# Performance work log

Hardware: AMD Instinct MI355X
Metric: run time of the kernel (lower is better)

## Reference

```python
import jax, jax.numpy as jnp
import numpy as np

B, S, D = 2, 2048, 1024
H, DH = 16, 64
LN_EPS = 1e-5
NEG_INF = -1e9


def setup_inputs() -> dict:
    key = jax.random.key(0)
    ks = jax.random.split(key, 8)
    x = jax.random.normal(ks[0], (B, S, D), dtype=jnp.float32)
    mask = jax.random.randint(ks[1], (B, 1, S, S), 0, 5) == 0
    sc = 1.0 / np.sqrt(D)
    W_attn = jax.random.normal(ks[2], (D, 3 * H * DH), dtype=jnp.float32) * sc
    b_attn = jnp.zeros((3 * H * DH,), dtype=jnp.float32)
    W_out = jax.random.normal(ks[3], (H * DH, D), dtype=jnp.float32) * sc
    b_out = jnp.zeros((D,), dtype=jnp.float32)
    ln_g = jnp.ones((D,), dtype=jnp.float32)
    ln_b = jnp.zeros((D,), dtype=jnp.float32)
    return {"x": x, "W_attn": W_attn, "b_attn": b_attn, "W_out": W_out,
            "b_out": b_out, "ln_g": ln_g, "ln_b": ln_b, "mask": mask}


def reference(x, W_attn, b_attn, W_out, b_out, ln_g, ln_b, mask):
    bs, s, _ = x.shape
    qkv = x @ W_attn + b_attn                      # [b, s, 3*H*DH]
    q, k, v = jnp.split(qkv, 3, axis=-1)
    q = q.reshape(bs, s, H, DH)
    k = k.reshape(bs, s, H, DH)
    v = v.reshape(bs, s, H, DH)
    scores = jnp.einsum('bqhd,bkhd->bhqk', q, k) / np.sqrt(DH)
    scores = jnp.where(mask, NEG_INF, scores)
    probs = jax.nn.softmax(scores, axis=-1)        # attn_p = 0 -> dropout is identity
    attn = jnp.einsum('bhqk,bkhd->bqhd', probs, v).reshape(bs, s, H * DH)
    y = x + (attn @ W_out + b_out)                 # resid_p = 0
    mu = jnp.mean(y, axis=-1, keepdims=True)
    var = jnp.mean((y - mu) ** 2, axis=-1, keepdims=True)
    return (y - mu) * jax.lax.rsqrt(var + LN_EPS) * ln_g + ln_b
```

## Files before the change

### kernel.cpp

```cpp
#include <hip/hip_runtime.h>
#include <math.h>

#define BB 2
#define SS 2048
#define DD 1024
#define HH 16
#define DHD 64
#define N3 3072
#define LN_EPS 1e-5f

#define PLANE (BB*HH*SS*DHD)

typedef __attribute__((ext_vector_type(8))) short bf16x8;
typedef __attribute__((ext_vector_type(4))) float f32x4;
typedef __attribute__((ext_vector_type(16))) float f32x16;
typedef unsigned int u32;
typedef unsigned short ushort_t;

static __device__ __forceinline__ short f2bf(float f) {
  union { float f; unsigned u; } a;
  a.f = f;
  unsigned r = a.u + 0x7fffu + ((a.u >> 16) & 1u);
  return (short)(r >> 16);
}

static __device__ __forceinline__ u32 fbits(float f) {
  union { float f; u32 u; } a; a.f = f; return a.u;
}

static __device__ __forceinline__ float ex2(float x) {
  float r;
  asm("v_exp_f32 %0, %1" : "=v"(r) : "v"(x));
  return r;
}

static __device__ __forceinline__ u32 pkbf(float lo, float hi) {
  return __builtin_amdgcn_perm(fbits(hi) + 0x8000u, fbits(lo) + 0x8000u,
                               0x07060302u);
}

static __device__ __forceinline__ void gload_lds16(const void* g, void* l) {
  __builtin_amdgcn_global_load_lds(
      (const __attribute__((address_space(1))) u32*)g,
      (__attribute__((address_space(3))) u32*)l, 16, 0, 0);
}

#define PREP_CONV_B   2048
#define PREP_TA_B     768
#define PREP_TO_B     256
#define PREP_PACK_B   32768
#define PREP_TOTAL_B  (PREP_CONV_B + PREP_TA_B + PREP_TO_B + PREP_PACK_B)

__global__ __launch_bounds__(256) void prep_kernel(
    const float* __restrict__ x, ushort_t* __restrict__ xb,
    const float* __restrict__ Wa, ushort_t* __restrict__ watt,
    const float* __restrict__ Wo, ushort_t* __restrict__ wot,
    const int* __restrict__ mask, unsigned long long* __restrict__ bits) {
  __shared__ float tile[64][65];
  const int tid = threadIdx.x;
  const int bid = blockIdx.x;

  if (bid < PREP_CONV_B) {
    int i = (bid * 256 + tid) * 8;
    float4 a = *(const float4*)&x[i];
    float4 b = *(const float4*)&x[i + 4];
    short s[8] = {f2bf(a.x), f2bf(a.y), f2bf(a.z), f2bf(a.w),
                  f2bf(b.x), f2bf(b.y), f2bf(b.z), f2bf(b.w)};
    *(bf16x8*)&xb[i] = *(bf16x8*)s;
    return;
  }
  if (bid < PREP_CONV_B + PREP_TA_B + PREP_TO_B) {
    const float* W; ushort_t* Wt; int K, N, nb, kb;
    if (bid < PREP_CONV_B + PREP_TA_B) {
      int idx = bid - PREP_CONV_B;
      W = Wa; Wt = watt; K = DD; N = N3;
      nb = (idx % 48) * 64; kb = (idx / 48) * 64;
    } else {
      int idx = bid - PREP_CONV_B - PREP_TA_B;
      W = Wo; Wt = wot; K = DD; N = DD;
      nb = (idx % 16) * 64; kb = (idx / 16) * 64;
    }
    #pragma unroll
    for (int i = 0; i < 4; ++i) {
      int idx = tid + i * 256;
      int r = idx >> 4, c = (idx & 15) * 4;
      float4 v = *(const float4*)&W[(size_t)(kb + r) * N + nb + c];
      tile[r][c] = v.x; tile[r][c + 1] = v.y;
      tile[r][c + 2] = v.z; tile[r][c + 3] = v.w;
    }
    __syncthreads();
    #pragma unroll
    for (int i = 0; i < 4; ++i) {
      int idx = tid + i * 256;
      int n = idx >> 4, k = (idx & 15) * 4;
      short4 s;
      s.x = f2bf(tile[k][n]); s.y = f2bf(tile[k + 1][n]);
      s.z = f2bf(tile[k + 2][n]); s.w = f2bf(tile[k + 3][n]);
      *(short4*)&Wt[(size_t)(nb + n) * K + kb + k] = s;
    }
    return;
  }
  {
    size_t g = (size_t)(bid - PREP_CONV_B - PREP_TA_B - PREP_TO_B) * 256 + tid;
    int m = mask[g];
    unsigned long long b = __ballot(m != 0);
    if ((tid & 63) == 0) bits[g >> 6] = b;
  }
}

#define GEMM_MAIN(Aptr, Btptr, Kdim)                                          \
  __shared__ ushort_t As[128 * 64];                                           \
  __shared__ ushort_t Bs[128 * 64];                                           \
  const int tid = threadIdx.x;                                                \
  const int wave = tid >> 6, lane = tid & 63;                                 \
  const int lane16 = lane & 15, quad = lane >> 4;                             \
  const int wm = wave & 1, wn = wave >> 1;                                    \
  const int bm = blockIdx.y * 128, bn = blockIdx.x * 128;                     \
  const int srow = lane >> 3;                                                 \
  const int sg = (lane & 7) ^ srow;                                           \
  f32x4 acc[4][4];                                                            \
  _Pragma("unroll") for (int i = 0; i < 4; ++i)                               \
    _Pragma("unroll") for (int j = 0; j < 4; ++j)                             \
      acc[i][j] = (f32x4){0.f, 0.f, 0.f, 0.f};                                \
  const ushort_t* agp[4];                                                     \
  const ushort_t* bgp[4];                                                     \
  _Pragma("unroll") for (int i = 0; i < 4; ++i) {                             \
    int seg = wave * 4 + i;                                                   \
    int r = seg * 8 + srow;                                                   \
    agp[i] = Aptr + (size_t)(bm + r) * Kdim + sg * 8;                         \
    bgp[i] = Btptr + (size_t)(bn + r) * Kdim + sg * 8;                        \
  }                                                                           \
  for (int k0 = 0; k0 < Kdim; k0 += 64) {                                     \
    _Pragma("unroll") for (int i = 0; i < 4; ++i) {                           \
      int seg = wave * 4 + i;                                                 \
      gload_lds16(agp[i] + k0, &As[seg * 512]);                               \
      gload_lds16(bgp[i] + k0, &Bs[seg * 512]);                               \
    }                                                                         \
    __syncthreads();                                                          \
    _Pragma("unroll") for (int ks = 0; ks < 2; ++ks) {                        \
      bf16x8 af[4], bfr[4];                                                   \
      _Pragma("unroll") for (int mt = 0; mt < 4; ++mt) {                      \
        int ra = wm * 64 + mt * 16 + lane16;                                  \
        int kc = ks * 4 + quad;                                               \
        af[mt] = *(const bf16x8*)&As[ra * 64 + ((kc ^ (ra & 7)) * 8)];        \
      }                                                                       \
      _Pragma("unroll") for (int nt = 0; nt < 4; ++nt) {                      \
        int rb = wn * 64 + nt * 16 + lane16;                                  \
        int kc = ks * 4 + quad;                                               \
        bfr[nt] = *(const bf16x8*)&Bs[rb * 64 + ((kc ^ (rb & 7)) * 8)];       \
      }                                                                       \
      _Pragma("unroll") for (int mt = 0; mt < 4; ++mt)                        \
        _Pragma("unroll") for (int nt = 0; nt < 4; ++nt)                      \
          acc[mt][nt] = __builtin_amdgcn_mfma_f32_16x16x32_bf16(              \
              af[mt], bfr[nt], acc[mt][nt], 0, 0, 0);                         \
    }                                                                         \
    __syncthreads();                                                          \
  }

__global__ __launch_bounds__(256) void gemm_qkv_mfma(
    const ushort_t* __restrict__ A, const ushort_t* __restrict__ Bt,
    const float* __restrict__ bias, ushort_t* __restrict__ qkvh) {
  GEMM_MAIN(A, Bt, DD)
  #pragma unroll
  for (int nt = 0; nt < 4; ++nt) {
    int col = bn + wn * 64 + nt * 16 + lane16;
    int which = col >> 10, hcol = col & 1023;
    int head = hcol >> 6, d = hcol & 63;
    float bv = bias[col];
    ushort_t* plane = qkvh + (size_t)which * PLANE;
    #pragma unroll
    for (int mt = 0; mt < 4; ++mt) {
      #pragma unroll
      for (int reg = 0; reg < 4; ++reg) {
        int row = bm + wm * 64 + mt * 16 + quad * 4 + reg;
        int bb = row >> 11, ss = row & (SS - 1);
        plane[((size_t)(bb * HH + head) * SS + ss) * DHD + d] =
            (ushort_t)f2bf(acc[mt][nt][reg] + bv);
      }
    }
  }
}

__global__ __launch_bounds__(256) void gemm_proj_mfma(
    const ushort_t* __restrict__ A, const ushort_t* __restrict__ Bt,
    const float* __restrict__ bias, const float* __restrict__ xres,
    float* __restrict__ Y) {
  GEMM_MAIN(A, Bt, DD)
  #pragma unroll
  for (int nt = 0; nt < 4; ++nt) {
    int col = bn + wn * 64 + nt * 16 + lane16;
    float bv = bias[col];
    #pragma unroll
    for (int mt = 0; mt < 4; ++mt) {
      #pragma unroll
      for (int reg = 0; reg < 4; ++reg) {
        int row = bm + wm * 64 + mt * 16 + quad * 4 + reg;
        Y[(size_t)row * DD + col] =
            acc[mt][nt][reg] + bv + xres[(size_t)row * DD + col];
      }
    }
  }
}

__global__ __launch_bounds__(256) void vtrans_kernel(
    const ushort_t* __restrict__ vh, ushort_t* __restrict__ vt) {
  __shared__ short t[64][80];
  const int tid = threadIdx.x;
  const int bh = blockIdx.x >> 5;
  const int st = blockIdx.x & 31;
  const size_t hb = (size_t)bh * SS * DHD;
  #pragma unroll
  for (int i = 0; i < 2; ++i) {
    int idx = tid + i * 256;
    int r = idx >> 3, ch = idx & 7;
    bf16x8 v = *(const bf16x8*)&vh[hb + (size_t)(st * 64 + r) * DHD + ch * 8];
    *(bf16x8*)&t[r][ch * 8] = v;
  }
  __syncthreads();
  #pragma unroll
  for (int i = 0; i < 2; ++i) {
    int idx = tid + i * 256;
    int d = idx >> 3, ch = idx & 7;
    short s[8];
    #pragma unroll
    for (int j = 0; j < 8; ++j) s[j] = t[ch * 8 + j][d];
    *(bf16x8*)&vt[hb + (size_t)d * SS + st * 64 + ch * 8] = *(bf16x8*)s;
  }
}

__global__ __launch_bounds__(512, 4) void attn_mfma_kernel(
    const ushort_t* __restrict__ qh, const ushort_t* __restrict__ kh,
    const ushort_t* __restrict__ vt, const u32* __restrict__ mbits,
    ushort_t* __restrict__ attn_out) {
  __shared__ __align__(16) ushort_t S[2][2][2][4096];

  const int tid = threadIdx.x;
  const int wave = tid >> 6, lane = tid & 63;
  const int l31 = lane & 31, hi = lane >> 5;

  const int bh = blockIdx.x & 31;
  const int qt = blockIdx.x >> 5;
  const int bbi = bh >> 4, hhi = bh & 15;
  const size_t head_base = (size_t)bh * SS * DHD;
  const int wq = wave & 3, khx = wave >> 2;
  const int q32 = qt * 128 + wq * 32;
  const int qrow = q32 + l31;

  bf16x8 qf[4];
  {
    const float kScale = 0.125f * 1.44269504f;
    const ushort_t* qsrc = &qh[head_base + (size_t)qrow * DHD + hi * 8];
    #pragma unroll
    for (int dk = 0; dk < 4; ++dk) {
      bf16x8 r = *(const bf16x8*)&qsrc[dk * 16];
      #pragma unroll
      for (int e = 0; e < 8; ++e) {
        union { u32 u; float f; } c;
        c.u = ((u32)(ushort_t)r[e]) << 16;
        c.f *= kScale;
        r[e] = f2bf(c.f);
      }
      qf[dk] = r;
    }
  }

  f32x16 acc0, acc1;
  #pragma unroll
  for (int e = 0; e < 16; ++e) { acc0[e] = 0.f; acc1[e] = 0.f; }
  float lsum = 0.f;

  const u32* mrow = mbits + ((size_t)(bbi * SS) + qrow) * 64 + khx * 32;

  const int sr = tid >> 3;
  const int scsrc = (tid & 7) ^ (sr & 7);
  const ushort_t* kst0 = kh + head_base + (size_t)sr * DHD + scsrc * 8;
  const ushort_t* vst0 = vt + head_base + (size_t)sr * SS + scsrc * 8;
  const int sdst = wave * 512;

#define ATTN_STAGE(buf, t)                                                    \
  gload_lds16(kst0 + (size_t)(t) * 64 * DHD, &S[buf][0][0][sdst]);            \
  gload_lds16(kst0 + (size_t)(1024 + (t) * 64) * DHD, &S[buf][0][1][sdst]);   \
  gload_lds16(vst0 + (t) * 64, &S[buf][1][0][sdst]);                          \
  gload_lds16(vst0 + 1024 + (t) * 64, &S[buf][1][1][sdst]);

  ATTN_STAGE(0, 0);
  uint2 mcur = *(const uint2*)mrow;
  __syncthreads();

  const int NT = 16;
  for (int t = 0; t < NT; ++t) {
    const int cur = t & 1;
    uint2 mnext = mcur;
    if (t + 1 < NT) {
      ATTN_STAGE(cur ^ 1, t + 1);
      mnext = *(const uint2*)&mrow[(t + 1) * 2];
    }

    const ushort_t* Kb = &S[cur][0][khx][0];
    const ushort_t* Vb = &S[cur][1][khx][0];

    f32x16 s0, s1;
    #pragma unroll
    for (int e = 0; e < 16; ++e) { s0[e] = 0.f; s1[e] = 0.f; }
    #pragma unroll
    for (int dk = 0; dk < 4; ++dk) {
      const int c = 2 * dk + hi;
      const int r0 = l31;
      bf16x8 kf0 = *(const bf16x8*)&Kb[r0 * 64 + ((c ^ (r0 & 7)) * 8)];
      s0 = __builtin_amdgcn_mfma_f32_32x32x16_bf16(kf0, qf[dk], s0, 0, 0, 0);
      const int r1 = 32 + l31;
      bf16x8 kf1 = *(const bf16x8*)&Kb[r1 * 64 + ((c ^ (r1 & 7)) * 8)];
      s1 = __builtin_amdgcn_mfma_f32_32x32x16_bf16(kf1, qf[dk], s1, 0, 0, 0);
    }

    #pragma unroll
    for (int ks16 = 0; ks16 < 4; ++ks16) {
      const int ksub = ks16 >> 1;
      const int g0 = (ks16 & 1) * 2;
      const f32x16 sv = ksub ? s1 : s0;
      const u32 w32 = ksub ? mcur.y : mcur.x;
      const u32 na = w32 >> (g0 * 8 + hi * 4);
      const u32 nb = w32 >> (g0 * 8 + 8 + hi * 4);
      float e0 = (na & 1u) ? 0.f : ex2(sv[g0 * 4 + 0]);
      float e1 = (na & 2u) ? 0.f : ex2(sv[g0 * 4 + 1]);
      float e2 = (na & 4u) ? 0.f : ex2(sv[g0 * 4 + 2]);
      float e3 = (na & 8u) ? 0.f : ex2(sv[g0 * 4 + 3]);
      float f0 = (nb & 1u) ? 0.f : ex2(sv[g0 * 4 + 4]);
      float f1 = (nb & 2u) ? 0.f : ex2(sv[g0 * 4 + 5]);
      float f2 = (nb & 4u) ? 0.f : ex2(sv[g0 * 4 + 6]);
      float f3 = (nb & 8u) ? 0.f : ex2(sv[g0 * 4 + 7]);
      lsum += ((e0 + e1) + (e2 + e3)) + ((f0 + f1) + (f2 + f3));
      u32 a0 = pkbf(e0, e1), a1 = pkbf(e2, e3);
      u32 b0 = pkbf(f0, f1), b1 = pkbf(f2, f3);
      asm("v_permlane32_swap_b32 %0, %1" : "+v"(a0), "+v"(b0));
      asm("v_permlane32_swap_b32 %0, %1" : "+v"(a1), "+v"(b1));
      union { u32 w[4]; bf16x8 v; } pfu;
      pfu.w[0] = a0; pfu.w[1] = a1; pfu.w[2] = b0; pfu.w[3] = b1;
      {
        const int rv0 = l31;
        const int cv = 2 * ks16 + hi;
        bf16x8 vf0 = *(const bf16x8*)&Vb[rv0 * 64 + ((cv ^ (rv0 & 7)) * 8)];
        acc0 = __builtin_amdgcn_mfma_f32_32x32x16_bf16(pfu.v, vf0, acc0, 0, 0, 0);
        const int rv1 = 32 + l31;
        bf16x8 vf1 = *(const bf16x8*)&Vb[rv1 * 64 + ((cv ^ (rv1 & 7)) * 8)];
        acc1 = __builtin_amdgcn_mfma_f32_32x32x16_bf16(pfu.v, vf1, acc1, 0, 0, 0);
      }
    }

    mcur = mnext;
    __syncthreads();
  }
#undef ATTN_STAGE

  float* mbuf = (float*)&S[0][0][0][0];
  float* lbuf = mbuf + 4 * 64 * 32;
  lbuf[((khx * 4 + wq) * 2 + hi) * 32 + l31] = lsum;
  if (khx == 1) {
    float* dst = mbuf + (size_t)(wq * 64 + lane) * 32;
    #pragma unroll
    for (int e = 0; e < 16; ++e) { dst[e] = acc0[e]; dst[16 + e] = acc1[e]; }
  }
  __syncthreads();
  if (khx == 0) {
    const float* src = mbuf + (size_t)(wq * 64 + lane) * 32;
    #pragma unroll
    for (int e = 0; e < 16; ++e) { acc0[e] += src[e]; acc1[e] += src[16 + e]; }
    #pragma unroll
    for (int reg = 0; reg < 16; ++reg) {
      const int kq = (reg & 3) + 8 * (reg >> 2) + 4 * hi;
      float lq = lbuf[((0 * 4 + wq) * 2 + 0) * 32 + kq]
               + lbuf[((0 * 4 + wq) * 2 + 1) * 32 + kq]
               + lbuf[((1 * 4 + wq) * 2 + 0) * 32 + kq]
               + lbuf[((1 * 4 + wq) * 2 + 1) * 32 + kq];
      const float inv = 1.0f / lq;
      ushort_t* orow = &attn_out[((size_t)(bbi * SS) + q32 + kq) * DD
                                 + hhi * DHD];
      orow[l31] = (ushort_t)f2bf(acc0[reg] * inv);
      orow[32 + l31] = (ushort_t)f2bf(acc1[reg] * inv);
    }
  }
}

__global__ __launch_bounds__(256) void ln_kernel(
    float* __restrict__ Y, const float* __restrict__ g,
    const float* __restrict__ bta) {
  const int r = blockIdx.x;
  const int tid = threadIdx.x;
  float4 v = *(const float4*)&Y[(size_t)r * DD + tid * 4];
  float sum = v.x + v.y + v.z + v.w;
  float sq = v.x * v.x + v.y * v.y + v.z * v.z + v.w * v.w;
  #pragma unroll
  for (int off = 32; off; off >>= 1) {
    sum += __shfl_down(sum, off);
    sq += __shfl_down(sq, off);
  }
  __shared__ float ps[4], pq[4];
  __shared__ float mu_s, rs_s;
  const int wave = tid >> 6;
  if ((tid & 63) == 0) { ps[wave] = sum; pq[wave] = sq; }
  __syncthreads();
  if (tid == 0) {
    float s = ps[0] + ps[1] + ps[2] + ps[3];
    float qq = pq[0] + pq[1] + pq[2] + pq[3];
    float mu = s * (1.0f / DD);
    float var = qq * (1.0f / DD) - mu * mu;
    mu_s = mu;
    rs_s = rsqrtf(var + LN_EPS);
  }
  __syncthreads();
  const float mu = mu_s, rs = rs_s;
  float4 g4 = *(const float4*)&g[tid * 4];
  float4 b4 = *(const float4*)&bta[tid * 4];
  float4 ov;
  ov.x = (v.x - mu) * rs * g4.x + b4.x;
  ov.y = (v.y - mu) * rs * g4.y + b4.y;
  ov.z = (v.z - mu) * rs * g4.z + b4.z;
  ov.w = (v.w - mu) * rs * g4.w + b4.w;
  *(float4*)&Y[(size_t)r * DD + tid * 4] = ov;
}

extern "C" void kernel_launch(void* const* d_in, const int* in_sizes, int n_in,
                              void* d_out, int out_size, void* d_ws, size_t ws_size,
                              hipStream_t stream) {
  const float* x      = (const float*)d_in[0];
  const float* W_attn = (const float*)d_in[1];
  const float* b_attn = (const float*)d_in[2];
  const float* W_out  = (const float*)d_in[3];
  const float* b_out  = (const float*)d_in[4];
  const float* ln_g   = (const float*)d_in[5];
  const float* ln_b   = (const float*)d_in[6];
  const int*   mask   = (const int*)d_in[7];
  float* out = (float*)d_out;
  ushort_t* ws = (ushort_t*)d_ws;

  ushort_t* xb    = ws;
  ushort_t* watt  = xb + (size_t)BB * SS * DD;
  ushort_t* wot   = watt + (size_t)N3 * DD;
  ushort_t* qh    = wot + (size_t)DD * DD;
  ushort_t* kh    = qh + (size_t)PLANE;
  ushort_t* vh    = kh + (size_t)PLANE;
  ushort_t* attnb = vh + (size_t)PLANE;
  u32* mbits      = (u32*)(attnb + (size_t)BB * SS * DD);
  ushort_t* vtb   = xb;

  prep_kernel<<<dim3(PREP_TOTAL_B), 256, 0, stream>>>(
      x, xb, W_attn, watt, W_out, wot, mask, (unsigned long long*)mbits);

  gemm_qkv_mfma<<<dim3(N3 / 128, (BB * SS) / 128), 256, 0, stream>>>(
      xb, watt, b_attn, qh);
  vtrans_kernel<<<dim3(BB * HH * (SS / 64)), 256, 0, stream>>>(vh, vtb);
  attn_mfma_kernel<<<dim3(BB * HH * (SS / 128)), 512, 0, stream>>>(
      qh, kh, vtb, mbits, attnb);
  gemm_proj_mfma<<<dim3(DD / 128, (BB * SS) / 128), 256, 0, stream>>>(
      attnb, wot, b_out, x, out);
  ln_kernel<<<dim3(BB * SS), 256, 0, stream>>>(out, ln_g, ln_b);
}
```

Before: 241.9 us.

## Fuse V transpose into QKV GEMM epilogue and unroll attention double-buffer loop

The QKV GEMM epilogue now writes V directly in transposed [b,h,d,s] layout, so the separate V-transpose kernel and its extra read/write pass are gone. The attention loop is unrolled by two with compile-time buffer indices and precomputed swizzled LDS addresses, which cuts per-tile address arithmetic. The reduction scratch buffer stride is padded from 32 to 33 floats to avoid LDS bank conflicts. The transposed epilogue stores are strided by SS in the sequence dimension, so they may coalesce poorly.

```diff
diff --git a/kernel.cpp b/kernel.cpp
--- a/kernel.cpp
+++ b/kernel.cpp
@@ -159,7 +159,8 @@
 
 __global__ __launch_bounds__(256) void gemm_qkv_mfma(
     const ushort_t* __restrict__ A, const ushort_t* __restrict__ Bt,
-    const float* __restrict__ bias, ushort_t* __restrict__ qkvh) {
+    const float* __restrict__ bias, ushort_t* __restrict__ qkvh,
+    ushort_t* __restrict__ vtb) {
   GEMM_MAIN(A, Bt, DD)
   #pragma unroll
   for (int nt = 0; nt < 4; ++nt) {
@@ -167,15 +168,28 @@
     int which = col >> 10, hcol = col & 1023;
     int head = hcol >> 6, d = hcol & 63;
     float bv = bias[col];
-    ushort_t* plane = qkvh + (size_t)which * PLANE;
-    #pragma unroll
-    for (int mt = 0; mt < 4; ++mt) {
+    if (which == 2) {
       #pragma unroll
-      for (int reg = 0; reg < 4; ++reg) {
-        int row = bm + wm * 64 + mt * 16 + quad * 4 + reg;
-        int bb = row >> 11, ss = row & (SS - 1);
-        plane[((size_t)(bb * HH + head) * SS + ss) * DHD + d] =
-            (ushort_t)f2bf(acc[mt][nt][reg] + bv);
+      for (int mt = 0; mt < 4; ++mt) {
+        #pragma unroll
+        for (int reg = 0; reg < 4; ++reg) {
+          int row = bm + wm * 64 + mt * 16 + quad * 4 + reg;
+          int bb = row >> 11, ss = row & (SS - 1);
+          vtb[((size_t)(bb * HH + head) * DHD + d) * SS + ss] =
+              (ushort_t)f2bf(acc[mt][nt][reg] + bv);
+        }
+      }
+    } else {
+      ushort_t* plane = qkvh + (size_t)which * PLANE;
+      #pragma unroll
+      for (int mt = 0; mt < 4; ++mt) {
+        #pragma unroll
+        for (int reg = 0; reg < 4; ++reg) {
+          int row = bm + wm * 64 + mt * 16 + quad * 4 + reg;
+          int bb = row >> 11, ss = row & (SS - 1);
+          plane[((size_t)(bb * HH + head) * SS + ss) * DHD + d] =
+              (ushort_t)f2bf(acc[mt][nt][reg] + bv);
+        }
       }
     }
   }
@@ -199,32 +213,6 @@
             acc[mt][nt][reg] + bv + xres[(size_t)row * DD + col];
       }
     }
-  }
-}
-
-__global__ __launch_bounds__(256) void vtrans_kernel(
-    const ushort_t* __restrict__ vh, ushort_t* __restrict__ vt) {
-  __shared__ short t[64][80];
-  const int tid = threadIdx.x;
-  const int bh = blockIdx.x >> 5;
-  const int st = blockIdx.x & 31;
-  const size_t hb = (size_t)bh * SS * DHD;
-  #pragma unroll
-  for (int i = 0; i < 2; ++i) {
-    int idx = tid + i * 256;
-    int r = idx >> 3, ch = idx & 7;
-    bf16x8 v = *(const bf16x8*)&vh[hb + (size_t)(st * 64 + r) * DHD + ch * 8];
-    *(bf16x8*)&t[r][ch * 8] = v;
-  }
-  __syncthreads();
-  #pragma unroll
-  for (int i = 0; i < 2; ++i) {
-    int idx = tid + i * 256;
-    int d = idx >> 3, ch = idx & 7;
-    short s[8];
-    #pragma unroll
-    for (int j = 0; j < 8; ++j) s[j] = t[ch * 8 + j][d];
-    *(bf16x8*)&vt[hb + (size_t)d * SS + st * 64 + ch * 8] = *(bf16x8*)s;
   }
 }
 
@@ -277,92 +265,93 @@
   const ushort_t* vst0 = vt + head_base + (size_t)sr * SS + scsrc * 8;
   const int sdst = wave * 512;
 
-#define ATTN_STAGE(buf, t)                                                    \
-  gload_lds16(kst0 + (size_t)(t) * 64 * DHD, &S[buf][0][0][sdst]);            \
-  gload_lds16(kst0 + (size_t)(1024 + (t) * 64) * DHD, &S[buf][0][1][sdst]);   \
-  gload_lds16(vst0 + (t) * 64, &S[buf][1][0][sdst]);                          \
-  gload_lds16(vst0 + 1024 + (t) * 64, &S[buf][1][1][sdst]);
-
-  ATTN_STAGE(0, 0);
+  const char* Sb = (const char*)&S[0][0][0][0];
+  const char* kaddr[4];
+  const char* vaddr[4];
+  #pragma unroll
+  for (int i = 0; i < 4; ++i) {
+    const int swzoff = (((2 * i + hi) ^ (l31 & 7)) * 16);
+    kaddr[i] = Sb + khx * 8192 + l31 * 128 + swzoff;
+    vaddr[i] = Sb + 16384 + khx * 8192 + l31 * 128 + swzoff;
+  }
+
+#define ATTN_STAGE(BUF, T)                                                    \
+  gload_lds16(kst0 + (size_t)(T) * 64 * DHD, &S[BUF][0][0][sdst]);            \
+  gload_lds16(kst0 + (size_t)(1024 + (T) * 64) * DHD, &S[BUF][0][1][sdst]);   \
+  gload_lds16(vst0 + (T) * 64, &S[BUF][1][0][sdst]);                          \
+  gload_lds16(vst0 + 1024 + (T) * 64, &S[BUF][1][1][sdst]);
+
+  ATTN_STAGE(0, 0)
   uint2 mcur = *(const uint2*)mrow;
   __syncthreads();
 
   const int NT = 16;
-  for (int t = 0; t < NT; ++t) {
-    const int cur = t & 1;
-    uint2 mnext = mcur;
-    if (t + 1 < NT) {
-      ATTN_STAGE(cur ^ 1, t + 1);
-      mnext = *(const uint2*)&mrow[(t + 1) * 2];
-    }
-
-    const ushort_t* Kb = &S[cur][0][khx][0];
-    const ushort_t* Vb = &S[cur][1][khx][0];
-
-    f32x16 s0, s1;
-    #pragma unroll
-    for (int e = 0; e < 16; ++e) { s0[e] = 0.f; s1[e] = 0.f; }
-    #pragma unroll
-    for (int dk = 0; dk < 4; ++dk) {
-      const int c = 2 * dk + hi;
-      const int r0 = l31;
-      bf16x8 kf0 = *(const bf16x8*)&Kb[r0 * 64 + ((c ^ (r0 & 7)) * 8)];
-      s0 = __builtin_amdgcn_mfma_f32_32x32x16_bf16(kf0, qf[dk], s0, 0, 0, 0);
-      const int r1 = 32 + l31;
-      bf16x8 kf1 = *(const bf16x8*)&Kb[r1 * 64 + ((c ^ (r1 & 7)) * 8)];
-      s1 = __builtin_amdgcn_mfma_f32_32x32x16_bf16(kf1, qf[dk], s1, 0, 0, 0);
-    }
-
-    #pragma unroll
-    for (int ks16 = 0; ks16 < 4; ++ks16) {
-      const int ksub = ks16 >> 1;
-      const int g0 = (ks16 & 1) * 2;
-      const f32x16 sv = ksub ? s1 : s0;
-      const u32 w32 = ksub ? mcur.y : mcur.x;
-      const u32 na = w32 >> (g0 * 8 + hi * 4);
-      const u32 nb = w32 >> (g0 * 8 + 8 + hi * 4);
-      float e0 = (na & 1u) ? 0.f : ex2(sv[g0 * 4 + 0]);
-      float e1 = (na & 2u) ? 0.f : ex2(sv[g0 * 4 + 1]);
-      float e2 = (na & 4u) ? 0.f : ex2(sv[g0 * 4 + 2]);
-      float e3 = (na & 8u) ? 0.f : ex2(sv[g0 * 4 + 3]);
-      float f0 = (nb & 1u) ? 0.f : ex2(sv[g0 * 4 + 4]);
-      float f1 = (nb & 2u) ? 0.f : ex2(sv[g0 * 4 + 5]);
-      float f2 = (nb & 4u) ? 0.f : ex2(sv[g0 * 4 + 6]);
-      float f3 = (nb & 8u) ? 0.f : ex2(sv[g0 * 4 + 7]);
-      lsum += ((e0 + e1) + (e2 + e3)) + ((f0 + f1) + (f2 + f3));
-      u32 a0 = pkbf(e0, e1), a1 = pkbf(e2, e3);
-      u32 b0 = pkbf(f0, f1), b1 = pkbf(f2, f3);
-      asm("v_permlane32_swap_b32 %0, %1" : "+v"(a0), "+v"(b0));
-      asm("v_permlane32_swap_b32 %0, %1" : "+v"(a1), "+v"(b1));
-      union { u32 w[4]; bf16x8 v; } pfu;
-      pfu.w[0] = a0; pfu.w[1] = a1; pfu.w[2] = b0; pfu.w[3] = b1;
-      {
-        const int rv0 = l31;
-        const int cv = 2 * ks16 + hi;
-        bf16x8 vf0 = *(const bf16x8*)&Vb[rv0 * 64 + ((cv ^ (rv0 & 7)) * 8)];
-        acc0 = __builtin_amdgcn_mfma_f32_32x32x16_bf16(pfu.v, vf0, acc0, 0, 0, 0);
-        const int rv1 = 32 + l31;
-        bf16x8 vf1 = *(const bf16x8*)&Vb[rv1 * 64 + ((cv ^ (rv1 & 7)) * 8)];
-        acc1 = __builtin_amdgcn_mfma_f32_32x32x16_bf16(pfu.v, vf1, acc1, 0, 0, 0);
-      }
-    }
-
-    mcur = mnext;
-    __syncthreads();
-  }
+
+#define ATTN_TILE(BUF, T)                                                     \
+  {                                                                           \
+    const int t_ = (T);                                                       \
+    uint2 mnext = mcur;                                                       \
+    if (t_ + 1 < NT) {                                                        \
+      ATTN_STAGE((BUF) ^ 1, t_ + 1)                                           \
+      mnext = *(const uint2*)&mrow[(t_ + 1) * 2];                             \
+    }                                                                         \
+    f32x16 s0, s1;                                                            \
+    _Pragma("unroll") for (int e = 0; e < 16; ++e) { s0[e] = 0.f; s1[e] = 0.f; } \
+    _Pragma("unroll") for (int dk = 0; dk < 4; ++dk) {                        \
+      bf16x8 kf0 = *(const bf16x8*)(kaddr[dk] + (BUF) * 32768);               \
+      s0 = __builtin_amdgcn_mfma_f32_32x32x16_bf16(kf0, qf[dk], s0, 0, 0, 0); \
+      bf16x8 kf1 = *(const bf16x8*)(kaddr[dk] + (BUF) * 32768 + 4096);        \
+      s1 = __builtin_amdgcn_mfma_f32_32x32x16_bf16(kf1, qf[dk], s1, 0, 0, 0); \
+    }                                                                         \
+    _Pragma("unroll") for (int ks16 = 0; ks16 < 4; ++ks16) {                  \
+      const int ksub = ks16 >> 1;                                             \
+      const int g0 = (ks16 & 1) * 2;                                          \
+      const f32x16 sv = ksub ? s1 : s0;                                       \
+      const u32 w32 = ksub ? mcur.y : mcur.x;                                 \
+      const u32 na = w32 >> (g0 * 8 + hi * 4);                                \
+      const u32 nb = w32 >> (g0 * 8 + 8 + hi * 4);                            \
+      float e0 = (na & 1u) ? 0.f : ex2(sv[g0 * 4 + 0]);                       \
+      float e1 = (na & 2u) ? 0.f : ex2(sv[g0 * 4 + 1]);                       \
+      float e2 = (na & 4u) ? 0.f : ex2(sv[g0 * 4 + 2]);                       \
+      float e3 = (na & 8u) ? 0.f : ex2(sv[g0 * 4 + 3]);                       \
+      float f0 = (nb & 1u) ? 0.f : ex2(sv[g0 * 4 + 4]);                       \
+      float f1 = (nb & 2u) ? 0.f : ex2(sv[g0 * 4 + 5]);                       \
+      float f2 = (nb & 4u) ? 0.f : ex2(sv[g0 * 4 + 6]);                       \
+      float f3 = (nb & 8u) ? 0.f : ex2(sv[g0 * 4 + 7]);                       \
+      lsum += ((e0 + e1) + (e2 + e3)) + ((f0 + f1) + (f2 + f3));              \
+      u32 a0 = pkbf(e0, e1), a1 = pkbf(e2, e3);                               \
+      u32 b0 = pkbf(f0, f1), b1 = pkbf(f2, f3);                               \
+      asm("v_permlane32_swap_b32 %0, %1" : "+v"(a0), "+v"(b0));               \
+      asm("v_permlane32_swap_b32 %0, %1" : "+v"(a1), "+v"(b1));               \
+      union { u32 w[4]; bf16x8 v; } pfu;                                      \
+      pfu.w[0] = a0; pfu.w[1] = a1; pfu.w[2] = b0; pfu.w[3] = b1;             \
+      bf16x8 vf0 = *(const bf16x8*)(vaddr[ks16] + (BUF) * 32768);             \
+      acc0 = __builtin_amdgcn_mfma_f32_32x32x16_bf16(pfu.v, vf0, acc0, 0, 0, 0); \
+      bf16x8 vf1 = *(const bf16x8*)(vaddr[ks16] + (BUF) * 32768 + 4096);      \
+      acc1 = __builtin_amdgcn_mfma_f32_32x32x16_bf16(pfu.v, vf1, acc1, 0, 0, 0); \
+    }                                                                         \
+    mcur = mnext;                                                             \
+    __syncthreads();                                                          \
+  }
+
+  for (int tt = 0; tt < NT; tt += 2) {
+    ATTN_TILE(0, tt)
+    ATTN_TILE(1, tt + 1)
+  }
+#undef ATTN_TILE
 #undef ATTN_STAGE
 
   float* mbuf = (float*)&S[0][0][0][0];
-  float* lbuf = mbuf + 4 * 64 * 32;
+  float* lbuf = mbuf + 4 * 64 * 33;
   lbuf[((khx * 4 + wq) * 2 + hi) * 32 + l31] = lsum;
   if (khx == 1) {
-    float* dst = mbuf + (size_t)(wq * 64 + lane) * 32;
+    float* dst = mbuf + (size_t)(wq * 64 + lane) * 33;
     #pragma unroll
     for (int e = 0; e < 16; ++e) { dst[e] = acc0[e]; dst[16 + e] = acc1[e]; }
   }
   __syncthreads();
   if (khx == 0) {
-    const float* src = mbuf + (size_t)(wq * 64 + lane) * 32;
+    const float* src = mbuf + (size_t)(wq * 64 + lane) * 33;
     #pragma unroll
     for (int e = 0; e < 16; ++e) { acc0[e] += src[e]; acc1[e] += src[16 + e]; }
     #pragma unroll
@@ -438,17 +427,15 @@
   ushort_t* wot   = watt + (size_t)N3 * DD;
   ushort_t* qh    = wot + (size_t)DD * DD;
   ushort_t* kh    = qh + (size_t)PLANE;
-  ushort_t* vh    = kh + (size_t)PLANE;
-  ushort_t* attnb = vh + (size_t)PLANE;
+  ushort_t* vtb   = kh + (size_t)PLANE;
+  ushort_t* attnb = vtb + (size_t)PLANE;
   u32* mbits      = (u32*)(attnb + (size_t)BB * SS * DD);
-  ushort_t* vtb   = xb;
 
   prep_kernel<<<dim3(PREP_TOTAL_B), 256, 0, stream>>>(
       x, xb, W_attn, watt, W_out, wot, mask, (unsigned long long*)mbits);
 
   gemm_qkv_mfma<<<dim3(N3 / 128, (BB * SS) / 128), 256, 0, stream>>>(
-      xb, watt, b_attn, qh);
-  vtrans_kernel<<<dim3(BB * HH * (SS / 64)), 256, 0, stream>>>(vh, vtb);
+      xb, watt, b_attn, qh, vtb);
   attn_mfma_kernel<<<dim3(BB * HH * (SS / 128)), 512, 0, stream>>>(
       qh, kh, vtb, mbits, attnb);
   gemm_proj_mfma<<<dim3(DD / 128, (BB * SS) / 128), 256, 0, stream>>>(
```

Result: slower. 262.4 us (+8.5%).

## Fuse V transpose into QKV GEMM epilogue and pad attention reduction buffer

Applied to the files above, without the earlier changes.

The QKV GEMM epilogue now writes the V columns straight into transposed [b,h,d,s] layout, so the separate vtrans kernel and the intermediate V plane round-trip go away. The attention kernel's cross-wave accumulator exchange buffer uses a row stride of 33 floats instead of 32, to avoid LDS bank conflicts. The transposed scalar stores write mostly consecutive ss within a lane's regs but strided across lanes, so V-store coalescing may be poorer than before.

```diff
diff --git a/kernel.cpp b/kernel.cpp
--- a/kernel.cpp
+++ b/kernel.cpp
@@ -159,7 +159,8 @@
 
 __global__ __launch_bounds__(256) void gemm_qkv_mfma(
     const ushort_t* __restrict__ A, const ushort_t* __restrict__ Bt,
-    const float* __restrict__ bias, ushort_t* __restrict__ qkvh) {
+    const float* __restrict__ bias, ushort_t* __restrict__ qkvh,
+    ushort_t* __restrict__ vtb) {
   GEMM_MAIN(A, Bt, DD)
   #pragma unroll
   for (int nt = 0; nt < 4; ++nt) {
@@ -167,15 +168,28 @@
     int which = col >> 10, hcol = col & 1023;
     int head = hcol >> 6, d = hcol & 63;
     float bv = bias[col];
-    ushort_t* plane = qkvh + (size_t)which * PLANE;
-    #pragma unroll
-    for (int mt = 0; mt < 4; ++mt) {
+    if (which == 2) {
       #pragma unroll
-      for (int reg = 0; reg < 4; ++reg) {
-        int row = bm + wm * 64 + mt * 16 + quad * 4 + reg;
-        int bb = row >> 11, ss = row & (SS - 1);
-        plane[((size_t)(bb * HH + head) * SS + ss) * DHD + d] =
-            (ushort_t)f2bf(acc[mt][nt][reg] + bv);
+      for (int mt = 0; mt < 4; ++mt) {
+        #pragma unroll
+        for (int reg = 0; reg < 4; ++reg) {
+          int row = bm + wm * 64 + mt * 16 + quad * 4 + reg;
+          int bb = row >> 11, ss = row & (SS - 1);
+          vtb[((size_t)(bb * HH + head) * DHD + d) * SS + ss] =
+              (ushort_t)f2bf(acc[mt][nt][reg] + bv);
+        }
+      }
+    } else {
+      ushort_t* plane = qkvh + (size_t)which * PLANE;
+      #pragma unroll
+      for (int mt = 0; mt < 4; ++mt) {
+        #pragma unroll
+        for (int reg = 0; reg < 4; ++reg) {
+          int row = bm + wm * 64 + mt * 16 + quad * 4 + reg;
+          int bb = row >> 11, ss = row & (SS - 1);
+          plane[((size_t)(bb * HH + head) * SS + ss) * DHD + d] =
+              (ushort_t)f2bf(acc[mt][nt][reg] + bv);
+        }
       }
     }
   }
@@ -199,32 +213,6 @@
             acc[mt][nt][reg] + bv + xres[(size_t)row * DD + col];
       }
     }
-  }
-}
-
-__global__ __launch_bounds__(256) void vtrans_kernel(
-    const ushort_t* __restrict__ vh, ushort_t* __restrict__ vt) {
-  __shared__ short t[64][80];
-  const int tid = threadIdx.x;
-  const int bh = blockIdx.x >> 5;
-  const int st = blockIdx.x & 31;
-  const size_t hb = (size_t)bh * SS * DHD;
-  #pragma unroll
-  for (int i = 0; i < 2; ++i) {
-    int idx = tid + i * 256;
-    int r = idx >> 3, ch = idx & 7;
-    bf16x8 v = *(const bf16x8*)&vh[hb + (size_t)(st * 64 + r) * DHD + ch * 8];
-    *(bf16x8*)&t[r][ch * 8] = v;
-  }
-  __syncthreads();
-  #pragma unroll
-  for (int i = 0; i < 2; ++i) {
-    int idx = tid + i * 256;
-    int d = idx >> 3, ch = idx & 7;
-    short s[8];
-    #pragma unroll
-    for (int j = 0; j < 8; ++j) s[j] = t[ch * 8 + j][d];
-    *(bf16x8*)&vt[hb + (size_t)d * SS + st * 64 + ch * 8] = *(bf16x8*)s;
   }
 }
 
@@ -353,16 +341,16 @@
 #undef ATTN_STAGE
 
   float* mbuf = (float*)&S[0][0][0][0];
-  float* lbuf = mbuf + 4 * 64 * 32;
+  float* lbuf = mbuf + 4 * 64 * 33;
   lbuf[((khx * 4 + wq) * 2 + hi) * 32 + l31] = lsum;
   if (khx == 1) {
-    float* dst = mbuf + (size_t)(wq * 64 + lane) * 32;
+    float* dst = mbuf + (size_t)(wq * 64 + lane) * 33;
     #pragma unroll
     for (int e = 0; e < 16; ++e) { dst[e] = acc0[e]; dst[16 + e] = acc1[e]; }
   }
   __syncthreads();
   if (khx == 0) {
-    const float* src = mbuf + (size_t)(wq * 64 + lane) * 32;
+    const float* src = mbuf + (size_t)(wq * 64 + lane) * 33;
     #pragma unroll
     for (int e = 0; e < 16; ++e) { acc0[e] += src[e]; acc1[e] += src[16 + e]; }
     #pragma unroll
@@ -438,17 +426,15 @@
   ushort_t* wot   = watt + (size_t)N3 * DD;
   ushort_t* qh    = wot + (size_t)DD * DD;
   ushort_t* kh    = qh + (size_t)PLANE;
-  ushort_t* vh    = kh + (size_t)PLANE;
-  ushort_t* attnb = vh + (size_t)PLANE;
+  ushort_t* vtb   = kh + (size_t)PLANE;
+  ushort_t* attnb = vtb + (size_t)PLANE;
   u32* mbits      = (u32*)(attnb + (size_t)BB * SS * DD);
-  ushort_t* vtb   = xb;
 
   prep_kernel<<<dim3(PREP_TOTAL_B), 256, 0, stream>>>(
       x, xb, W_attn, watt, W_out, wot, mask, (unsigned long long*)mbits);
 
   gemm_qkv_mfma<<<dim3(N3 / 128, (BB * SS) / 128), 256, 0, stream>>>(
-      xb, watt, b_attn, qh);
-  vtrans_kernel<<<dim3(BB * HH * (SS / 64)), 256, 0, stream>>>(vh, vtb);
+      xb, watt, b_attn, qh, vtb);
   attn_mfma_kernel<<<dim3(BB * HH * (SS / 128)), 512, 0, stream>>>(
       qh, kh, vtb, mbits, attnb);
   gemm_proj_mfma<<<dim3(DD / 128, (BB * SS) / 128), 256, 0, stream>>>(
```

Result: faster. 233.3 us (-3.6%).
